# Kernel optimization log

Hardware: AMD Instinct MI355X
Metric: run time of the kernel (lower is better)

## Reference

```python
import jax, jax.numpy as jnp
import numpy as np

N_NODES = 50000
N_EDGES = 1600000


def gcn_conv(h, W, b, src, dst, ew, n_nodes):
    """PyG GCNConv: linear -> add self-loops (weight 1) -> sym-norm scatter-add -> bias."""
    h = h @ W                                   # [N, out]
    loop = jnp.arange(n_nodes, dtype=src.dtype)
    s = jnp.concatenate([src, loop])            # [E+N]
    d = jnp.concatenate([dst, loop])
    w = jnp.concatenate([ew, jnp.ones((n_nodes,), dtype=h.dtype)])
    deg = jax.ops.segment_sum(w, d, num_segments=n_nodes)          # in-degree (weighted)
    dinv = jnp.where(deg > 0, jax.lax.rsqrt(deg), 0.0)
    coef = dinv[s] * w * dinv[d]                # D^-1/2 A D^-1/2 per-edge coefficient
    msg = h[s] * coef[:, None]                  # gather + scale  [E+N, out]
    out = jax.ops.segment_sum(msg, d, num_segments=n_nodes)        # scatter-add
    return out + b


def setup_inputs() -> dict:
    key = jax.random.key(0)
    ks = jax.random.split(key, 6)
    x = jax.random.normal(ks[0], (N_NODES, 256), dtype=jnp.float32)
    edge_index = jax.random.randint(ks[1], (2, N_EDGES), 0, N_NODES, dtype=jnp.int64)
    edge_weight = jax.random.uniform(ks[2], (N_EDGES,), dtype=jnp.float32)
    W1 = jax.random.normal(ks[3], (256, 128), dtype=jnp.float32) * (1.0 / np.sqrt(256))
    b1 = jnp.zeros((128,), dtype=jnp.float32)
    W2 = jax.random.normal(ks[4], (128, 64), dtype=jnp.float32) * (1.0 / np.sqrt(128))
    b2 = jnp.zeros((64,), dtype=jnp.float32)
    return {"x": x, "edge_index": edge_index, "edge_weight": edge_weight,
            "W1": W1, "b1": b1, "W2": W2, "b2": b2}


def reference(x, edge_index, edge_weight, W1, b1, W2, b2):
    src, dst = edge_index[0], edge_index[1]
    n = x.shape[0]
    h = gcn_conv(x, W1, b1, src, dst, edge_weight, n)
    h = jax.nn.relu(h)
    # dropout is identity in eval mode
    out = gcn_conv(h, W2, b2, src, dst, edge_weight, n)
    return out
```

## Files before the change

kernel.cpp:

```cpp
#include <hip/hip_runtime.h>

#define NN 50000
#define NE 1600000
#define NB 391
#define NBLK 512
#define EPB 3125
#define CAP 4992

typedef short bf16x8 __attribute__((ext_vector_type(8)));
typedef float f32x4 __attribute__((ext_vector_type(4)));

static __device__ __forceinline__ unsigned f2bf(float f) {
    union { float f; unsigned u; } v; v.f = f;
    return (v.u + 0x7FFF + ((v.u >> 16) & 1)) >> 16;
}

static __device__ __forceinline__ void accq(float* acc, float& cs, uint2 g, float c) {
    cs += c;
    acc[0] += (float)(g.x & 0xffu) * c;
    acc[1] += (float)((g.x >> 8) & 0xffu) * c;
    acc[2] += (float)((g.x >> 16) & 0xffu) * c;
    acc[3] += (float)(g.x >> 24) * c;
    acc[4] += (float)(g.y & 0xffu) * c;
    acc[5] += (float)((g.y >> 8) & 0xffu) * c;
    acc[6] += (float)((g.y >> 16) & 0xffu) * c;
    acc[7] += (float)(g.y >> 24) * c;
}

__global__ __launch_bounds__(256) void k1_scatter(const int* __restrict__ src,
        const int* __restrict__ dst, const float* __restrict__ ew,
        int* __restrict__ cursor, int2* __restrict__ ebuf,
        const float* __restrict__ W1, const float* __restrict__ W2,
        const float* __restrict__ b1,
        ushort* __restrict__ Wt1, ushort* __restrict__ Wt2,
        float* __restrict__ b1p) {
    int blk = blockIdx.x;
    int t = threadIdx.x;
    if (blk >= NBLK) {
        for (int idx = (blk - NBLK) * 256 + t; idx < 41088; idx += 32 * 256) {
            if (idx < 32768) {
                int k = idx >> 7, n = idx & 127;
                Wt1[n * 256 + k] = (ushort)f2bf(W1[idx]);
            } else if (idx < 40960) {
                int i = idx - 32768;
                int k = i >> 6, n = i & 63;
                int kp = ((k & 15) << 3) | (k >> 4);
                Wt2[n * 128 + kp] = (ushort)f2bf(W2[i]);
            } else {
                int k = idx - 40960;
                b1p[((k & 15) << 3) | (k >> 4)] = b1[k];
            }
        }
        return;
    }
    __shared__ int h[NB];
    __shared__ int curs[NB];
    __shared__ int sdst[EPB];
    for (int i = t; i < NB; i += 256) h[i] = 0;
    __syncthreads();
    int base = blk * EPB;
    for (int k = t; k < EPB; k += 256) {
        int d = dst[base + k];
        sdst[k] = d;
        atomicAdd(&h[d >> 7], 1);
    }
    __syncthreads();
    for (int i = t; i < NB; i += 256)
        curs[i] = i * CAP + atomicAdd(&cursor[i], h[i]);
    __syncthreads();
    for (int k = t; k < EPB; k += 256) {
        int d = sdst[k];
        int s = src[base + k];
        float w = ew[base + k];
        int pos = atomicAdd(&curs[d >> 7], 1);
        ebuf[pos] = make_int2(s | ((d & 127) << 16), __float_as_int(w));
    }
}

__global__ __launch_bounds__(512) void p4_build(const int2* __restrict__ ebuf,
        const int* __restrict__ cursor, unsigned* __restrict__ edata,
        float* __restrict__ dinv, int2* __restrict__ rowptr2) {
    __shared__ int cnt[128], loff[128], cur[128], sd[128];
    __shared__ float deg[128];
    __shared__ int2 se[CAP];
    int bk = blockIdx.x;
    int t = threadIdx.x;
    int ebase = bk * CAP;
    int ecnt = cursor[bk];
    if (ecnt > CAP) ecnt = CAP;
    if (t < 128) { cnt[t] = 0; cur[t] = 0; deg[t] = 0.0f; }
    __syncthreads();
    for (int i = t; i < ecnt; i += 512) {
        int2 e = ebuf[ebase + i];
        se[i] = e;
        int dl = (e.x >> 16) & 127;
        atomicAdd(&cnt[dl], 1);
        atomicAdd(&deg[dl], __int_as_float(e.y));
    }
    __syncthreads();
    if (t < 128) sd[t] = (cnt[t] + 3) & ~3;
    __syncthreads();
    for (int off = 1; off < 128; off <<= 1) {
        int v = 0;
        if (t < 128 && t >= off) v = sd[t - off];
        __syncthreads();
        if (t < 128) sd[t] += v;
        __syncthreads();
    }
    if (t < 128) {
        int cp = (cnt[t] + 3) & ~3;
        loff[t] = sd[t] - cp;
    }
    __syncthreads();
    int node = bk * 128 + t;
    if (t < 128 && node < NN) {
        dinv[node] = rsqrtf(deg[t] + 1.0f);
        int cp = (cnt[t] + 3) & ~3;
        int beg = ebase + loff[t];
        rowptr2[node] = make_int2(beg, beg + cp);
        for (int i = cnt[t]; i < cp; ++i)
            edata[ebase + loff[t] + i] = 0;
    }
    for (int i = t; i < ecnt; i += 512) {
        int2 e = se[i];
        int dl = (e.x >> 16) & 127;
        int slot = loff[dl] + atomicAdd(&cur[dl], 1);
        edata[ebase + slot] = (unsigned)(e.x & 0xFFFF)
                            | (f2bf(__int_as_float(e.y)) << 16);
    }
}

__global__ __launch_bounds__(256) void gemm1_kernel(const float* __restrict__ A,
        const ushort* __restrict__ Bt, unsigned char* __restrict__ H1q,
        float* __restrict__ sscale, const float* __restrict__ dinv, int M) {
    const int K = 256;
    __shared__ __align__(16) ushort As[64][72];
    __shared__ __align__(16) ushort Bs[128][72];
    int tid = threadIdx.x;
    int bm = blockIdx.x * 64;
    int w = tid >> 6, lane = tid & 63;
    int m = lane & 15, quad = lane >> 4;
    f32x4 acc[8] = {};
    int ra = tid >> 2, ksa = (tid & 3) * 16;
    int rb = tid >> 1, ksb = (tid & 1) * 32;
    int grow = bm + ra; if (grow >= M) grow = M - 1;
    const float* ap = A + (size_t)grow * K + ksa;
    const ushort* bp = Bt + (size_t)rb * K + ksb;
    for (int k0 = 0; k0 < K; k0 += 64) {
        float4 f0 = *(const float4*)(ap + k0);
        float4 f1 = *(const float4*)(ap + k0 + 4);
        float4 f2 = *(const float4*)(ap + k0 + 8);
        float4 f3 = *(const float4*)(ap + k0 + 12);
        uint4 bv0 = *(const uint4*)(bp + k0);
        uint4 bv1 = *(const uint4*)(bp + k0 + 8);
        uint4 bv2 = *(const uint4*)(bp + k0 + 16);
        uint4 bv3 = *(const uint4*)(bp + k0 + 24);
        uint4 pa, pb;
        pa.x = f2bf(f0.x) | (f2bf(f0.y) << 16);
        pa.y = f2bf(f0.z) | (f2bf(f0.w) << 16);
        pa.z = f2bf(f1.x) | (f2bf(f1.y) << 16);
        pa.w = f2bf(f1.z) | (f2bf(f1.w) << 16);
        pb.x = f2bf(f2.x) | (f2bf(f2.y) << 16);
        pb.y = f2bf(f2.z) | (f2bf(f2.w) << 16);
        pb.z = f2bf(f3.x) | (f2bf(f3.y) << 16);
        pb.w = f2bf(f3.z) | (f2bf(f3.w) << 16);
        __syncthreads();
        *(uint4*)&As[ra][ksa] = pa;
        *(uint4*)&As[ra][ksa + 8] = pb;
        *(uint4*)&Bs[rb][ksb] = bv0;
        *(uint4*)&Bs[rb][ksb + 8] = bv1;
        *(uint4*)&Bs[rb][ksb + 16] = bv2;
        *(uint4*)&Bs[rb][ksb + 24] = bv3;
        __syncthreads();
        #pragma unroll
        for (int ks = 0; ks < 2; ++ks) {
            bf16x8 a = *(const bf16x8*)&As[w * 16 + m][ks * 32 + quad * 8];
            #pragma unroll
            for (int t = 0; t < 8; ++t) {
                bf16x8 b = *(const bf16x8*)&Bs[t * 16 + m][ks * 32 + quad * 8];
                acc[t] = __builtin_amdgcn_mfma_f32_16x16x32_bf16(a, b, acc[t], 0, 0, 0);
            }
        }
    }
    int rbase = bm + w * 16 + quad * 4;
    float dv[4];
    #pragma unroll
    for (int rg = 0; rg < 4; ++rg)
        dv[rg] = (rbase + rg < M) ? dinv[rbase + rg] : 0.0f;
    #pragma unroll
    for (int rg = 0; rg < 4; ++rg) {
        float val[8];
        float mx = 0.0f;
        #pragma unroll
        for (int t = 0; t < 8; ++t) {
            val[t] = dv[rg] * acc[t][rg];
            mx = fmaxf(mx, fabsf(val[t]));
        }
        #pragma unroll
        for (int off = 1; off < 16; off <<= 1)
            mx = fmaxf(mx, __shfl_xor(mx, off));
        float s = mx * (1.0f / 127.0f);
        float inv = (mx > 0.0f) ? 127.0f / mx : 0.0f;
        unsigned d0 = 0, d1 = 0;
        #pragma unroll
        for (int t = 0; t < 4; ++t) {
            unsigned q0 = (unsigned)(__float2int_rn(val[t] * inv) + 128);
            unsigned q1 = (unsigned)(__float2int_rn(val[t + 4] * inv) + 128);
            d0 |= (q0 & 255u) << (8 * t);
            d1 |= (q1 & 255u) << (8 * t);
        }
        int row = rbase + rg;
        if (row < M) {
            *(uint2*)&H1q[(size_t)row * 128 + m * 8] = make_uint2(d0, d1);
            if (m == 0) sscale[row] = s;
        }
    }
}

__global__ __launch_bounds__(256) void fix_edata(const unsigned* __restrict__ edata,
        const float* __restrict__ scale, unsigned* __restrict__ eout, int total) {
    int i = blockIdx.x * 256 + threadIdx.x;
    if (i >= total) return;
    unsigned e = edata[i];
    float w = __uint_as_float(e & 0xFFFF0000u);
    float c = w * scale[e & 0xFFFF];
    eout[i] = (e & 0xFFFFu) | (f2bf(c) << 16);
}

__global__ __launch_bounds__(256) void agg1_fused_kernel(
        const int2* __restrict__ rowptr2, const unsigned* __restrict__ edata1,
        const unsigned char* __restrict__ Hq, const float* __restrict__ sscale,
        const float* __restrict__ dinv, const float* __restrict__ b1p,
        const ushort* __restrict__ Wt2, unsigned char* __restrict__ H2q,
        float* __restrict__ sscale2) {
    __shared__ __align__(16) ushort Ats[16][136];
    __shared__ int rmax[16];
    __shared__ unsigned char Hq2s[16][64];
    int tid = threadIdx.x;
    int nl = tid >> 4;
    int node = blockIdx.x * 16 + nl;
    int glane = tid & 15;
    int2 rp = rowptr2[node];
    int beg = rp.x, end = rp.y;
    float acc[8] = {};
    float cs = 0.0f;
    const unsigned char* Hql = Hq + glane * 8;
    int e = beg;
    int n8 = beg + ((end - beg) & ~7);
    for (; e < n8; e += 8) {
        uint4 ma = *(const uint4*)&edata1[e];
        uint4 mb = *(const uint4*)&edata1[e + 4];
        uint2 g0 = *(const uint2*)(Hql + (size_t)(ma.x & 0xFFFF) * 128);
        uint2 g1 = *(const uint2*)(Hql + (size_t)(ma.y & 0xFFFF) * 128);
        uint2 g2 = *(const uint2*)(Hql + (size_t)(ma.z & 0xFFFF) * 128);
        uint2 g3 = *(const uint2*)(Hql + (size_t)(ma.w & 0xFFFF) * 128);
        uint2 g4 = *(const uint2*)(Hql + (size_t)(mb.x & 0xFFFF) * 128);
        uint2 g5 = *(const uint2*)(Hql + (size_t)(mb.y & 0xFFFF) * 128);
        uint2 g6 = *(const uint2*)(Hql + (size_t)(mb.z & 0xFFFF) * 128);
        uint2 g7 = *(const uint2*)(Hql + (size_t)(mb.w & 0xFFFF) * 128);
        accq(acc, cs, g0, __uint_as_float(ma.x & 0xFFFF0000u));
        accq(acc, cs, g1, __uint_as_float(ma.y & 0xFFFF0000u));
        accq(acc, cs, g2, __uint_as_float(ma.z & 0xFFFF0000u));
        accq(acc, cs, g3, __uint_as_float(ma.w & 0xFFFF0000u));
        accq(acc, cs, g4, __uint_as_float(mb.x & 0xFFFF0000u));
        accq(acc, cs, g5, __uint_as_float(mb.y & 0xFFFF0000u));
        accq(acc, cs, g6, __uint_as_float(mb.z & 0xFFFF0000u));
        accq(acc, cs, g7, __uint_as_float(mb.w & 0xFFFF0000u));
    }
    if (e < end) {
        uint4 ma = *(const uint4*)&edata1[e];
        uint2 g0 = *(const uint2*)(Hql + (size_t)(ma.x & 0xFFFF) * 128);
        uint2 g1 = *(const uint2*)(Hql + (size_t)(ma.y & 0xFFFF) * 128);
        uint2 g2 = *(const uint2*)(Hql + (size_t)(ma.z & 0xFFFF) * 128);
        uint2 g3 = *(const uint2*)(Hql + (size_t)(ma.w & 0xFFFF) * 128);
        accq(acc, cs, g0, __uint_as_float(ma.x & 0xFFFF0000u));
        accq(acc, cs, g1, __uint_as_float(ma.y & 0xFFFF0000u));
        accq(acc, cs, g2, __uint_as_float(ma.z & 0xFFFF0000u));
        accq(acc, cs, g3, __uint_as_float(ma.w & 0xFFFF0000u));
    }
    {
        float ss = sscale[node];
        uint2 gs = *(const uint2*)(Hql + (size_t)node * 128);
        accq(acc, cs, gs, ss);
    }
    float di = dinv[node];
    float corr = -128.0f * cs;
    float4 bv0 = *(const float4*)(b1p + glane * 8);
    float4 bv1 = *(const float4*)(b1p + glane * 8 + 4);
    float v[8];
    #pragma unroll
    for (int j = 0; j < 8; ++j) v[j] = di * (acc[j] + corr);
    v[0] += bv0.x; v[1] += bv0.y; v[2] += bv0.z; v[3] += bv0.w;
    v[4] += bv1.x; v[5] += bv1.y; v[6] += bv1.z; v[7] += bv1.w;
    #pragma unroll
    for (int k = 0; k < 8; ++k) v[k] = fmaxf(v[k], 0.0f);
    uint4 o;
    o.x = f2bf(v[0]) | (f2bf(v[1]) << 16);
    o.y = f2bf(v[2]) | (f2bf(v[3]) << 16);
    o.z = f2bf(v[4]) | (f2bf(v[5]) << 16);
    o.w = f2bf(v[6]) | (f2bf(v[7]) << 16);
    *(uint4*)&Ats[nl][glane * 8] = o;
    if (tid < 16) rmax[tid] = 0;
    __syncthreads();
    int w = tid >> 6, lane = tid & 63;
    int m = lane & 15, quad = lane >> 4;
    const ushort* bp = Wt2 + (size_t)(w * 16 + m) * 128 + quad * 8;
    f32x4 c2 = {};
    #pragma unroll
    for (int kc = 0; kc < 4; ++kc) {
        bf16x8 a = *(const bf16x8*)&Ats[m][kc * 32 + quad * 8];
        bf16x8 b = *(const bf16x8*)(bp + kc * 32);
        c2 = __builtin_amdgcn_mfma_f32_16x16x32_bf16(a, b, c2, 0, 0, 0);
    }
    int rl = quad * 4;
    float val[4];
    #pragma unroll
    for (int rg = 0; rg < 4; ++rg) {
        float dvr = dinv[blockIdx.x * 16 + rl + rg];
        val[rg] = dvr * c2[rg];
        float a = fabsf(val[rg]);
        a = fmaxf(a, __shfl_xor(a, 1));
        a = fmaxf(a, __shfl_xor(a, 2));
        a = fmaxf(a, __shfl_xor(a, 4));
        a = fmaxf(a, __shfl_xor(a, 8));
        if (m == 0) atomicMax(&rmax[rl + rg], __float_as_int(a));
    }
    __syncthreads();
    #pragma unroll
    for (int rg = 0; rg < 4; ++rg) {
        float mx = __int_as_float(rmax[rl + rg]);
        float inv = (mx > 0.0f) ? 127.0f / mx : 0.0f;
        unsigned q = (unsigned)(__float2int_rn(val[rg] * inv) + 128);
        Hq2s[rl + rg][w * 16 + m] = (unsigned char)q;
        if (w == 0 && m == 0)
            sscale2[blockIdx.x * 16 + rl + rg] = mx * (1.0f / 127.0f);
    }
    __syncthreads();
    ((unsigned*)H2q)[blockIdx.x * 256 + tid] = ((const unsigned*)Hq2s)[tid];
}

__global__ __launch_bounds__(256) void agg2_kernel(
        const int2* __restrict__ rowptr2, const unsigned* __restrict__ edata2,
        const unsigned char* __restrict__ Hq, const float* __restrict__ sscale2,
        const float* __restrict__ dinv, const float* __restrict__ bias,
        float* __restrict__ out) {
    int node = blockIdx.x * 32 + (threadIdx.x >> 3);
    if (node >= NN) return;
    int glane = threadIdx.x & 7;
    int2 rp = rowptr2[node];
    int beg = rp.x, end = rp.y;
    float acc[8] = {};
    float cs = 0.0f;
    const unsigned char* Hql = Hq + glane * 8;
    int e = beg;
    int n8 = beg + ((end - beg) & ~7);
    for (; e < n8; e += 8) {
        uint4 ma = *(const uint4*)&edata2[e];
        uint4 mb = *(const uint4*)&edata2[e + 4];
        uint2 g0 = *(const uint2*)(Hql + (size_t)(ma.x & 0xFFFF) * 64);
        uint2 g1 = *(const uint2*)(Hql + (size_t)(ma.y & 0xFFFF) * 64);
        uint2 g2 = *(const uint2*)(Hql + (size_t)(ma.z & 0xFFFF) * 64);
        uint2 g3 = *(const uint2*)(Hql + (size_t)(ma.w & 0xFFFF) * 64);
        uint2 g4 = *(const uint2*)(Hql + (size_t)(mb.x & 0xFFFF) * 64);
        uint2 g5 = *(const uint2*)(Hql + (size_t)(mb.y & 0xFFFF) * 64);
        uint2 g6 = *(const uint2*)(Hql + (size_t)(mb.z & 0xFFFF) * 64);
        uint2 g7 = *(const uint2*)(Hql + (size_t)(mb.w & 0xFFFF) * 64);
        accq(acc, cs, g0, __uint_as_float(ma.x & 0xFFFF0000u));
        accq(acc, cs, g1, __uint_as_float(ma.y & 0xFFFF0000u));
        accq(acc, cs, g2, __uint_as_float(ma.z & 0xFFFF0000u));
        accq(acc, cs, g3, __uint_as_float(ma.w & 0xFFFF0000u));
        accq(acc, cs, g4, __uint_as_float(mb.x & 0xFFFF0000u));
        accq(acc, cs, g5, __uint_as_float(mb.y & 0xFFFF0000u));
        accq(acc, cs, g6, __uint_as_float(mb.z & 0xFFFF0000u));
        accq(acc, cs, g7, __uint_as_float(mb.w & 0xFFFF0000u));
    }
    if (e < end) {
        uint4 ma = *(const uint4*)&edata2[e];
        uint2 g0 = *(const uint2*)(Hql + (size_t)(ma.x & 0xFFFF) * 64);
        uint2 g1 = *(const uint2*)(Hql + (size_t)(ma.y & 0xFFFF) * 64);
        uint2 g2 = *(const uint2*)(Hql + (size_t)(ma.z & 0xFFFF) * 64);
        uint2 g3 = *(const uint2*)(Hql + (size_t)(ma.w & 0xFFFF) * 64);
        accq(acc, cs, g0, __uint_as_float(ma.x & 0xFFFF0000u));
        accq(acc, cs, g1, __uint_as_float(ma.y & 0xFFFF0000u));
        accq(acc, cs, g2, __uint_as_float(ma.z & 0xFFFF0000u));
        accq(acc, cs, g3, __uint_as_float(ma.w & 0xFFFF0000u));
    }
    {
        float ss = sscale2[node];
        uint2 gs = *(const uint2*)(Hql + (size_t)node * 64);
        accq(acc, cs, gs, ss);
    }
    float di = dinv[node];
    float corr = -128.0f * cs;
    float4 bv0 = *(const float4*)(bias + glane * 8);
    float4 bv1 = *(const float4*)(bias + glane * 8 + 4);
    float v[8];
    #pragma unroll
    for (int j = 0; j < 8; ++j) v[j] = di * (acc[j] + corr);
    v[0] += bv0.x; v[1] += bv0.y; v[2] += bv0.z; v[3] += bv0.w;
    v[4] += bv1.x; v[5] += bv1.y; v[6] += bv1.z; v[7] += bv1.w;
    float* o = out + (size_t)node * 64 + glane * 8;
    *(float4*)(o)     = make_float4(v[0], v[1], v[2], v[3]);
    *(float4*)(o + 4) = make_float4(v[4], v[5], v[6], v[7]);
}

extern "C" void kernel_launch(void* const* d_in, const int* in_sizes, int n_in,
                              void* d_out, int out_size, void* d_ws, size_t ws_size,
                              hipStream_t stream) {
    const float* x  = (const float*)d_in[0];
    const int*   ei = (const int*)d_in[1];
    const float* ew = (const float*)d_in[2];
    const float* W1 = (const float*)d_in[3];
    const float* b1 = (const float*)d_in[4];
    const float* W2 = (const float*)d_in[5];
    const float* b2 = (const float*)d_in[6];
    const int* src = ei;
    const int* dst = ei + NE;
    float* out = (float*)d_out;

    float*  ws      = (float*)d_ws;
    float*  dinv    = ws;
    int2*   rowptr2 = (int2*)(ws + 50048);
    int*    cursor  = (int*)(ws + 150144);
    ushort* Wt1     = (ushort*)(ws + 150656);
    ushort* Wt2     = (ushort*)(ws + 167040);
    float*  b1p     = ws + 171136;
    float*  sscale  = ws + 171264;
    float*  sscale2 = ws + 221312;
    unsigned* edata = (unsigned*)(ws + 271360);
    unsigned* edata1= (unsigned*)(ws + 2223232);
    unsigned* edata2= (unsigned*)(ws + 4175104);
    unsigned char* H1q = (unsigned char*)(ws + 6126976);
    unsigned char* H2q = (unsigned char*)(ws + 7726976);
    int2*   ebuf    = (int2*)edata1;

    hipMemsetAsync(cursor, 0, NB * sizeof(int), stream);
    k1_scatter<<<NBLK + 32, 256, 0, stream>>>(src, dst, ew, cursor, ebuf,
                                              W1, W2, b1, Wt1, Wt2, b1p);
    p4_build<<<NB, 512, 0, stream>>>(ebuf, cursor, edata, dinv, rowptr2);

    gemm1_kernel<<<782, 256, 0, stream>>>(x, Wt1, H1q, sscale, dinv, NN);
    fix_edata<<<(NB * CAP + 255) / 256, 256, 0, stream>>>(edata, sscale, edata1,
                                                          NB * CAP);
    agg1_fused_kernel<<<3125, 256, 0, stream>>>(rowptr2, edata1, H1q, sscale,
                                                dinv, b1p, Wt2, H2q, sscale2);
    fix_edata<<<(NB * CAP + 255) / 256, 256, 0, stream>>>(edata, sscale2, edata2,
                                                          NB * CAP);
    agg2_kernel<<<1563, 256, 0, stream>>>(rowptr2, edata2, H2q, sscale2,
                                          dinv, b2, out);
}
```

Before: 236.8 us.

## Stage edge bucketing in shared memory for coalesced global writes

The edge-binning kernel now computes a local prefix sum of bucket counts, scatters each edge into a shared-memory buffer ordered by bucket, and then writes the buffer to global memory contiguously per bucket, so the global stores are close to coalesced instead of random. The number of edges per block drops from 3125 to 2000 and the block count rises from 512 to 800 so the larger shared-memory footprint fits. The bucket id is packed into the high bits of the edge word. The extra scan and synchronisation add overhead, and the wider packed word assumes source indices fit in 16 bits.

```diff
diff --git a/kernel.cpp b/kernel.cpp
--- a/kernel.cpp
+++ b/kernel.cpp
@@ -3,8 +3,8 @@
 #define NN 50000
 #define NE 1600000
 #define NB 391
-#define NBLK 512
-#define EPB 3125
+#define NBLK 800
+#define EPB 2000
 #define CAP 4992
 
 typedef short bf16x8 __attribute__((ext_vector_type(8)));
@@ -54,8 +54,11 @@
         return;
     }
     __shared__ int h[NB];
+    __shared__ int sd[512];
     __shared__ int curs[NB];
+    __shared__ int gofs[NB];
     __shared__ int sdst[EPB];
+    __shared__ int2 sebuf[EPB];
     for (int i = t; i < NB; i += 256) h[i] = 0;
     __syncthreads();
     int base = blk * EPB;
@@ -65,15 +68,38 @@
         atomicAdd(&h[d >> 7], 1);
     }
     __syncthreads();
-    for (int i = t; i < NB; i += 256)
-        curs[i] = i * CAP + atomicAdd(&cursor[i], h[i]);
+    sd[t] = (t < NB) ? h[t] : 0;
+    sd[t + 256] = (t + 256 < NB) ? h[t + 256] : 0;
+    __syncthreads();
+    for (int off = 1; off < 512; off <<= 1) {
+        int v0 = (t >= off) ? sd[t - off] : 0;
+        int v1 = sd[t + 256 - off];
+        __syncthreads();
+        if (t >= off) sd[t] += v0;
+        sd[t + 256] += v1;
+        __syncthreads();
+    }
+    for (int i = t; i < NB; i += 256) {
+        int lofs = sd[i] - h[i];
+        curs[i] = lofs;
+        int gb = i * CAP + atomicAdd(&cursor[i], h[i]);
+        gofs[i] = gb - lofs;
+    }
     __syncthreads();
     for (int k = t; k < EPB; k += 256) {
         int d = sdst[k];
         int s = src[base + k];
         float w = ew[base + k];
-        int pos = atomicAdd(&curs[d >> 7], 1);
-        ebuf[pos] = make_int2(s | ((d & 127) << 16), __float_as_int(w));
+        int b = d >> 7;
+        int slot = atomicAdd(&curs[b], 1);
+        sebuf[slot] = make_int2(s | ((d & 127) << 16) | (b << 23),
+                                __float_as_int(w));
+    }
+    __syncthreads();
+    for (int i = t; i < EPB; i += 256) {
+        int2 e = sebuf[i];
+        int b = ((unsigned)e.x) >> 23;
+        ebuf[gofs[b] + i] = e;
     }
 }
 
```

New measurement: 242.0 us. 1.02x slower.
